# Optimization experiments

Measured on AMD Instinct MI355X. Metric: run time of the kernel, lower is better.

Reference implementation:

```python
import jax, jax.numpy as jnp
import numpy as np

QLEN, B, D, NH, DH, DI = 1024, 4, 1024, 16, 64, 4096
KLEN = QLEN
RLEN = QLEN + KLEN
EPS = 1e-12
SCALE = 1.0 / (DH ** 0.5)


def layer_norm(x, g, b):
    mu = jnp.mean(x, axis=-1, keepdims=True)
    var = jnp.mean(jnp.square(x - mu), axis=-1, keepdims=True)
    return (x - mu) * jax.lax.rsqrt(var + EPS) * g + b


def rel_shift(x, klen):
    # x: [qlen, rlen, b, n] -> [qlen, klen, b, n] via XLNet reshape trick
    q, r_, b, n = x.shape
    x = jnp.reshape(x, (r_, q, b, n))[1:]
    x = jnp.reshape(x, (q, r_ - 1, b, n))[:, :klen]
    return x


def setup_inputs() -> dict:
    key = jax.random.key(0)
    ks = jax.random.split(key, 16)
    std = 0.02
    h = jax.random.normal(ks[0], (QLEN, B, D), jnp.float32)
    r = jax.random.normal(ks[1], (RLEN, B, D), jnp.float32)
    # causal mask: 1 where key position j > query position i (disallowed)
    m = (jnp.arange(KLEN)[None, :] > jnp.arange(QLEN)[:, None]).astype(jnp.float32)
    attn_mask = jnp.broadcast_to(m[:, :, None, None], (QLEN, KLEN, B, 1))
    # segment matrix: one-hot of (seg_i != seg_j), shape [q, k, b, 2]
    seg_ids = jax.random.randint(ks[2], (QLEN, B), 0, 2)
    diff = (seg_ids[:, None, :] != seg_ids[None, :, :]).astype(jnp.int32)
    seg_mat = jax.nn.one_hot(diff, 2, dtype=jnp.float32)
    p = lambda k, shape: jax.random.normal(k, shape, jnp.float32) * std
    return {
        'h': h, 'r': r, 'attn_mask': attn_mask, 'seg_mat': seg_mat,
        'q_w': p(ks[3], (D, NH, DH)), 'k_w': p(ks[4], (D, NH, DH)),
        'v_w': p(ks[5], (D, NH, DH)), 'o_w': p(ks[6], (D, NH, DH)),
        'r_w': p(ks[7], (D, NH, DH)),
        'r_r_bias': jnp.zeros((NH, DH), jnp.float32),
        'r_s_bias': jnp.zeros((NH, DH), jnp.float32),
        'r_w_bias': jnp.zeros((NH, DH), jnp.float32),
        'seg_embed': p(ks[8], (2, NH, DH)),
        'ln1_g': jnp.ones((D,), jnp.float32), 'ln1_b': jnp.zeros((D,), jnp.float32),
        'ff_w1': p(ks[9], (D, DI)), 'ff_b1': jnp.zeros((DI,), jnp.float32),
        'ff_w2': p(ks[10], (DI, D)), 'ff_b2': jnp.zeros((D,), jnp.float32),
        'ln2_g': jnp.ones((D,), jnp.float32), 'ln2_b': jnp.zeros((D,), jnp.float32),
    }


def reference(h, r, attn_mask, seg_mat, q_w, k_w, v_w, o_w, r_w,
              r_r_bias, r_s_bias, r_w_bias, seg_embed,
              ln1_g, ln1_b, ff_w1, ff_b1, ff_w2, ff_b2, ln2_g, ln2_b):
    # projections (single-stream: g=None, mems=None => cat == h)
    q_head = jnp.einsum('ibh,hnd->ibnd', h, q_w)
    k_head = jnp.einsum('ibh,hnd->ibnd', h, k_w)
    v_head = jnp.einsum('ibh,hnd->ibnd', h, v_w)
    k_r = jnp.einsum('ibh,hnd->ibnd', r, r_w)
    # content + relative position + segment bias terms
    ac = jnp.einsum('ibnd,jbnd->ijbn', q_head + r_w_bias, k_head)
    bd = jnp.einsum('ibnd,jbnd->ijbn', q_head + r_r_bias, k_r)
    bd = rel_shift(bd, KLEN)
    ef = jnp.einsum('ibnd,snd->ibns', q_head + r_s_bias, seg_embed)
    ef = jnp.einsum('ijbs,ibns->ijbn', seg_mat, ef)
    attn_score = (ac + bd + ef) * SCALE - 1e30 * attn_mask
    attn_prob = jax.nn.softmax(attn_score, axis=1)
    attn_vec = jnp.einsum('ijbn,jbnd->ibnd', attn_prob, v_head)
    # post-attention
    attn_out = jnp.einsum('ibnd,hnd->ibh', attn_vec, o_w) + h
    out = layer_norm(attn_out, ln1_g, ln1_b)
    # feed-forward
    ff = jax.nn.gelu(jnp.einsum('ibh,hf->ibf', out, ff_w1) + ff_b1, approximate=False)
    ff = jnp.einsum('ibf,fh->ibh', ff, ff_w2) + ff_b2
    return layer_norm(ff + out, ln2_g, ln2_b)
```

## Files before the change

kernel.cpp:

```cpp
#include <hip/hip_runtime.h>
#include <hip/hip_bf16.h>

using bf16 = __hip_bfloat16;
typedef __attribute__((ext_vector_type(8))) short short8;
typedef __attribute__((ext_vector_type(4))) float floatx4;

#define QLEN 1024
#define KLEN 1024
#define RLEN 2048
#define RUSED 1152
#define BB   4
#define DMODEL 1024
#define NH   16
#define DH   64
#define DI   4096
#define ND   1024
#define QKVS 3072
#define SCALE 0.125f

__device__ inline void gl_lds16(const bf16* g, bf16* l) {
  __builtin_amdgcn_global_load_lds(
      (__attribute__((address_space(1))) void*)(g),
      (__attribute__((address_space(3))) void*)(l), 16, 0, 0);
}

__global__ __launch_bounds__(256) void cvt_all(
    const float* __restrict__ h, const float* __restrict__ r,
    const float* __restrict__ ow,
    bf16* __restrict__ hb, bf16* __restrict__ rb, bf16* __restrict__ wo)
{
  const int id = blockIdx.x;
  const float* src; bf16* dst; int off;
  if (id < 2048)      { src = h;  dst = hb; off = id * 2048; }
  else if (id < 4352) { src = r;  dst = rb; off = (id - 2048) * 2048; }
  else                { src = ow; dst = wo; off = (id - 4352) * 2048; }
  const int idx = off + threadIdx.x * 8;
  const float4 a = *reinterpret_cast<const float4*>(src + idx);
  const float4 b = *reinterpret_cast<const float4*>(src + idx + 4);
  bf16 o[8] = {__float2bfloat16(a.x), __float2bfloat16(a.y),
               __float2bfloat16(a.z), __float2bfloat16(a.w),
               __float2bfloat16(b.x), __float2bfloat16(b.y),
               __float2bfloat16(b.z), __float2bfloat16(b.w)};
  *reinterpret_cast<uint4*>(dst + idx) = *reinterpret_cast<uint4*>(o);
}

__device__ inline void tconv_tile(const float* __restrict__ src, bf16* __restrict__ dst,
                                  int R, int C, int bx, int by, int tid) {
  __shared__ float tile[32][33];
  const int r0 = by * 32, c0 = bx * 32;
  {
    const int tr = tid >> 3, tc = (tid & 7) * 4;
    const float4 f = *reinterpret_cast<const float4*>(src + (size_t)(r0 + tr) * C + c0 + tc);
    tile[tr][tc + 0] = f.x; tile[tr][tc + 1] = f.y;
    tile[tr][tc + 2] = f.z; tile[tr][tc + 3] = f.w;
  }
  __syncthreads();
  {
    const int oc = tid >> 3, orr = (tid & 7) * 4;
    bf16 o[4];
#pragma unroll
    for (int u = 0; u < 4; ++u) o[u] = __float2bfloat16(tile[orr + u][oc]);
    *reinterpret_cast<uint2*>(dst + (size_t)(c0 + oc) * R + r0 + orr) = *reinterpret_cast<uint2*>(o);
  }
}

__global__ __launch_bounds__(256) void tconv_all(
    const float* __restrict__ qw, const float* __restrict__ kw,
    const float* __restrict__ vw, const float* __restrict__ rw,
    const float* __restrict__ w1, const float* __restrict__ w2,
    bf16* __restrict__ wqkvt, bf16* __restrict__ wrt,
    bf16* __restrict__ w1t, bf16* __restrict__ w2t)
{
  const int id = blockIdx.x;
  const int tid = threadIdx.x;
  if (id < 4096) {
    const int part = id >> 10, local = id & 1023;
    const float* src = (part == 0) ? qw : (part == 1) ? kw : (part == 2) ? vw : rw;
    bf16* dst = (part < 3) ? (wqkvt + (size_t)part * ND * DMODEL) : wrt;
    tconv_tile(src, dst, DMODEL, ND, local & 31, local >> 5, tid);
  } else if (id < 8192) {
    const int local = id - 4096;
    tconv_tile(w1, w1t, DMODEL, DI, local & 127, local >> 7, tid);
  } else {
    const int local = id - 8192;
    tconv_tile(w2, w2t, DI, DMODEL, local & 31, local >> 5, tid);
  }
}

__global__ __launch_bounds__(256) void seg_extract(const float* __restrict__ seg,
                                                   float* __restrict__ dsb) {
  const int idx = blockIdx.x * 256 + threadIdx.x;
  const int i = idx >> 2, b = idx & 3;
  dsb[b * QLEN + i] = seg[(size_t)(i * KLEN * BB + b) * 2 + 1];
}

__global__ __launch_bounds__(512, 4) void gemm256(
    const bf16* __restrict__ A, const bf16* __restrict__ Bt,
    int M, int N, int K, int Ktot, int lda, int ldb,
    const float* __restrict__ bias, int act_gelu,
    float* __restrict__ outf, bf16* __restrict__ outb, int pstride)
{
  __shared__ __attribute__((aligned(16))) bf16 As[2][128 * 64];
  __shared__ __attribute__((aligned(16))) bf16 Bs[2][128 * 64];

  const int tid = threadIdx.x;
  const int wave = tid >> 6, lane = tid & 63;

  const int gX = gridDim.x;
  const int nwg = gX * gridDim.y;
  int lin = blockIdx.y * gX + blockIdx.x;
  {
    const int q = nwg >> 3, r = nwg & 7;
    const int xcd = lin & 7, idx = lin >> 3;
    lin = (xcd < r ? xcd * (q + 1) : r * (q + 1) + (xcd - r) * q) + idx;
  }
  const int n0b = (lin % gX) << 7;
  const int m0b = (lin / gX) << 7;

  const int z = blockIdx.z;
  const int kbeg = z * K;
  const int nkt = min(K, Ktot - kbeg) >> 6;
  const bf16* Ab = A + (size_t)kbeg;
  const bf16* Bb = Bt + (size_t)kbeg;
  float* of = outf ? (outf + (size_t)z * pstride) : outf;
  bf16*  ob = outb ? (outb + (size_t)z * pstride) : outb;

  const int srow = lane >> 3;
  const int scol = ((lane & 7) ^ srow) << 3;
  const bf16* gA = Ab + (size_t)(m0b + wave * 8 + srow) * lda + scol;
  const bf16* gB = Bb + (size_t)(n0b + wave * 8 + srow) * ldb + scol;
  const int lofs = wave * (8 * 64) + lane * 8;
  bf16* lA[2] = {&As[0][lofs], &As[1][lofs]};
  bf16* lB[2] = {&Bs[0][lofs], &Bs[1][lofs]};

  const int fl = lane & 15, quad = lane >> 4;
  const int wm = (wave >> 2) * 64;
  const int wn = (wave & 3) * 32;
  const int ch0 = (quad ^ (fl & 7)) << 3;

  floatx4 acc[4][2];
#pragma unroll
  for (int mi = 0; mi < 4; ++mi)
#pragma unroll
    for (int ni = 0; ni < 2; ++ni) acc[mi][ni] = (floatx4){0.f, 0.f, 0.f, 0.f};

  {
    gl_lds16(gA, lA[0]);
    gl_lds16(gA + (size_t)64 * lda, lA[0] + 4096);
    gl_lds16(gB, lB[0]);
    gl_lds16(gB + (size_t)64 * ldb, lB[0] + 4096);
  }
  if (nkt > 1) {
    gl_lds16(gA + 64, lA[1]);
    gl_lds16(gA + (size_t)64 * lda + 64, lA[1] + 4096);
    gl_lds16(gB + 64, lB[1]);
    gl_lds16(gB + (size_t)64 * ldb + 64, lB[1] + 4096);
  }

  for (int kt = 0; kt < nkt; ++kt) {
    if (kt + 1 < nkt) {
      asm volatile("s_waitcnt vmcnt(4)" ::: "memory");
    } else {
      asm volatile("s_waitcnt vmcnt(0)" ::: "memory");
    }
    __builtin_amdgcn_s_barrier();
    __builtin_amdgcn_sched_barrier(0);

    const bf16* as = (kt & 1) ? &As[1][0] : &As[0][0];
    const bf16* bs = (kt & 1) ? &Bs[1][0] : &Bs[0][0];
#pragma unroll
    for (int ks = 0; ks < 2; ++ks) {
      const int ch = ch0 ^ (ks << 5);
      short8 af[4], bv[2];
#pragma unroll
      for (int mi = 0; mi < 4; ++mi)
        af[mi] = *reinterpret_cast<const short8*>(&as[(wm + mi * 16 + fl) * 64 + ch]);
#pragma unroll
      for (int ni = 0; ni < 2; ++ni)
        bv[ni] = *reinterpret_cast<const short8*>(&bs[(wn + ni * 16 + fl) * 64 + ch]);
      __builtin_amdgcn_s_setprio(1);
#pragma unroll
      for (int mi = 0; mi < 4; ++mi)
#pragma unroll
        for (int ni = 0; ni < 2; ++ni)
          acc[mi][ni] = __builtin_amdgcn_mfma_f32_16x16x32_bf16(af[mi], bv[ni], acc[mi][ni], 0, 0, 0);
      __builtin_amdgcn_s_setprio(0);
    }
    __builtin_amdgcn_sched_barrier(0);
    __builtin_amdgcn_s_barrier();
    if (kt + 2 < nkt) {
      const size_t ko = (size_t)(kt + 2) << 6;
      bf16* dA = (kt & 1) ? lA[1] : lA[0];
      bf16* dB = (kt & 1) ? lB[1] : lB[0];
      gl_lds16(gA + ko, dA);
      gl_lds16(gA + (size_t)64 * lda + ko, dA + 4096);
      gl_lds16(gB + ko, dB);
      gl_lds16(gB + (size_t)64 * ldb + ko, dB + 4096);
    }
  }

#pragma unroll
  for (int mi = 0; mi < 4; ++mi) {
#pragma unroll
    for (int r = 0; r < 4; ++r) {
      const int row = m0b + wm + mi * 16 + quad * 4 + r;
#pragma unroll
      for (int ni = 0; ni < 2; ++ni) {
        const int col = n0b + wn + ni * 16 + fl;
        float v = acc[mi][ni][r];
        if (bias) v += bias[col];
        if (act_gelu) v = 0.5f * v * (1.0f + erff(v * 0.70710678118654752f));
        const size_t idx = (size_t)row * N + col;
        if (of) of[idx] = v;
        else    ob[idx] = __float2bfloat16(v);
      }
    }
  }
}

__global__ __launch_bounds__(256, 3) void attn_kernel(
    const bf16* __restrict__ qkv, const bf16* __restrict__ kr,
    const float* __restrict__ dsb, const float* __restrict__ seg_embed,
    const float* __restrict__ rwb, const float* __restrict__ rrb,
    const float* __restrict__ rsb,
    bf16* __restrict__ av_out)
{
  const int bx = blockIdx.x;
  const int n  = bx & 15;
  const int b  = (bx >> 4) & 3;
  const int it = 15 - (bx >> 6);
  const int i0 = it * 64;
  const int tid = threadIdx.x;

  const bf16* qh = qkv + n * DH;
  const bf16* kh = qkv + ND + n * DH;
  const bf16* vh = qkv + 2 * ND + n * DH;

  __shared__ bf16 Kb[64][72];
  __shared__ bf16 VT[64][72];
  __shared__ bf16 krw[128][72];
  __shared__ bf16 bdrL[64][88];
  __shared__ float efs0[64], efs1[64];
  __shared__ float dsq[64], dsk[64];

  const int wave = tid >> 6, lane = tid & 63;
  const int fl = lane & 15, quad = lane >> 4;
  const int wq0 = wave * 16;
  const int tb0 = 3 - wave;
  const int twoc = (tid & 3) << 1;

  short8 aw[2], ar[2];
  {
    const int qrow = i0 + wq0 + fl;
    const bf16* qp = qh + (size_t)(qrow * BB + b) * QKVS;
    float e0 = 0.f, e1 = 0.f;
#pragma unroll
    for (int ks = 0; ks < 2; ++ks) {
      const int d0 = ks * 32 + quad * 8;
      const uint4 qv = *reinterpret_cast<const uint4*>(qp + d0);
      const bf16* qe = reinterpret_cast<const bf16*>(&qv);
      bf16 wt[8], rt[8];
#pragma unroll
      for (int u = 0; u < 8; ++u) {
        const int d = d0 + u;
        const float qf = __bfloat162float(qe[u]);
        wt[u] = __float2bfloat16(qf + rwb[n * DH + d]);
        rt[u] = __float2bfloat16(qf + rrb[n * DH + d]);
        const float qs = qf + rsb[n * DH + d];
        e0 += qs * seg_embed[(0 * NH + n) * DH + d];
        e1 += qs * seg_embed[(1 * NH + n) * DH + d];
      }
      aw[ks] = *reinterpret_cast<short8*>(wt);
      ar[ks] = *reinterpret_cast<short8*>(rt);
    }
    e0 += __shfl_xor(e0, 16, 64); e0 += __shfl_xor(e0, 32, 64);
    e1 += __shfl_xor(e1, 16, 64); e1 += __shfl_xor(e1, 32, 64);
    if (quad == 0) { efs0[wq0 + fl] = e0; efs1[wq0 + fl] = e1; }
    if (tid < 64) dsq[tid] = dsb[b * QLEN + i0 + tid];
  }

  floatx4 O[4];
#pragma unroll
  for (int nb = 0; nb < 4; ++nb) O[nb] = (floatx4){0.f, 0.f, 0.f, 0.f};
  float l_loc[4] = {0.f, 0.f, 0.f, 0.f};

  const int sj  = tid >> 2;
  const int sdc = (tid & 3) << 4;
  const int st  = tid >> 1;
  const int sdc2= (tid & 1) << 5;
  uint4 kv0, kv1, vv0, vv1, rr0, rr1, rr2, rr3;
  {
    const bf16* kp = kh + (size_t)((0 + sj) * BB + b) * QKVS + sdc;
    kv0 = reinterpret_cast<const uint4*>(kp)[0];
    kv1 = reinterpret_cast<const uint4*>(kp)[1];
    const bf16* vp = vh + (size_t)((0 + sj) * BB + b) * QKVS + sdc;
    vv0 = reinterpret_cast<const uint4*>(vp)[0];
    vv1 = reinterpret_cast<const uint4*>(vp)[1];
    const int kbase0 = QLEN - i0 - 63;
    const bf16* rp = kr + ((size_t)((kbase0 + st) * BB + b)) * ND + n * DH + sdc2;
    rr0 = reinterpret_cast<const uint4*>(rp)[0];
    rr1 = reinterpret_cast<const uint4*>(rp)[1];
    rr2 = reinterpret_cast<const uint4*>(rp)[2];
    rr3 = reinterpret_cast<const uint4*>(rp)[3];
  }

  for (int jt = 0; jt <= it; ++jt) {
    const int j0 = jt * 64;

    __syncthreads();

    {
      reinterpret_cast<uint4*>(&Kb[sj][sdc])[0] = kv0;
      reinterpret_cast<uint4*>(&Kb[sj][sdc + 8])[0] = kv1;
      const bf16* ve0 = reinterpret_cast<const bf16*>(&vv0);
      const bf16* ve1 = reinterpret_cast<const bf16*>(&vv1);
#pragma unroll
      for (int u = 0; u < 8; ++u) {
        VT[sdc + (u ^ twoc)][sj] = ve0[u];
        VT[sdc + 8 + (u ^ twoc)][sj] = ve1[u];
      }
      reinterpret_cast<uint4*>(&krw[st][sdc2 + 0])[0]  = rr0;
      reinterpret_cast<uint4*>(&krw[st][sdc2 + 8])[0]  = rr1;
      reinterpret_cast<uint4*>(&krw[st][sdc2 + 16])[0] = rr2;
      reinterpret_cast<uint4*>(&krw[st][sdc2 + 24])[0] = rr3;
      if (tid < 64) dsk[tid] = dsb[b * QLEN + j0 + tid];
    }

    if (jt < it) {
      const int j0n = j0 + 64;
      const bf16* kp = kh + (size_t)((j0n + sj) * BB + b) * QKVS + sdc;
      kv0 = reinterpret_cast<const uint4*>(kp)[0];
      kv1 = reinterpret_cast<const uint4*>(kp)[1];
      const bf16* vp = vh + (size_t)((j0n + sj) * BB + b) * QKVS + sdc;
      vv0 = reinterpret_cast<const uint4*>(vp)[0];
      vv1 = reinterpret_cast<const uint4*>(vp)[1];
      const int kbn = QLEN + j0n - i0 - 63;
      const bf16* rp = kr + ((size_t)((kbn + st) * BB + b)) * ND + n * DH + sdc2;
      rr0 = reinterpret_cast<const uint4*>(rp)[0];
      rr1 = reinterpret_cast<const uint4*>(rp)[1];
      rr2 = reinterpret_cast<const uint4*>(rp)[2];
      rr3 = reinterpret_cast<const uint4*>(rp)[3];
    }

    __syncthreads();

    floatx4 accS[4], accB[5];
#pragma unroll
    for (int nb = 0; nb < 4; ++nb) accS[nb] = (floatx4){0.f, 0.f, 0.f, 0.f};
#pragma unroll
    for (int u = 0; u < 5; ++u) accB[u] = (floatx4){0.f, 0.f, 0.f, 0.f};
#pragma unroll
    for (int ks = 0; ks < 2; ++ks) {
#pragma unroll
      for (int nb = 0; nb < 4; ++nb)
        accS[nb] = __builtin_amdgcn_mfma_f32_16x16x32_bf16(
            aw[ks], *reinterpret_cast<const short8*>(&Kb[nb * 16 + fl][ks * 32 + quad * 8]), accS[nb], 0, 0, 0);
#pragma unroll
      for (int u = 0; u < 5; ++u)
        accB[u] = __builtin_amdgcn_mfma_f32_16x16x32_bf16(
            ar[ks], *reinterpret_cast<const short8*>(&krw[(tb0 + u) * 16 + fl][ks * 32 + quad * 8]), accB[u], 0, 0, 0);
    }
#pragma unroll
    for (int u = 0; u < 5; ++u)
#pragma unroll
      for (int r = 0; r < 4; ++r)
        bdrL[wq0 + quad * 4 + r][u * 16 + fl] = __float2bfloat16(accB[u][r]);

    float pv[4][4];
#pragma unroll
    for (int r = 0; r < 4; ++r) {
      const int qL = wq0 + quad * 4 + r;
      const int qg = i0 + qL;
      const float e0q = efs0[qL], e1q = efs1[qL];
      const float dq = dsq[qL];
#pragma unroll
      for (int nb = 0; nb < 4; ++nb) {
        const int kL = nb * 16 + fl;
        const int kg = j0 + kL;
        const float bdv = __bfloat162float(bdrL[qL][15 + kL - quad * 4 - r]);
        const float ef = (dq != dsk[kL]) ? e1q : e0q;
        const float s = (accS[nb][r] + bdv + ef) * SCALE;
        const float pe = (kg > qg) ? 0.0f : __expf(s);
        pv[nb][r] = pe;
        l_loc[r] += pe;
      }
    }

#pragma unroll
    for (int nb = 0; nb < 4; ++nb)
#pragma unroll
      for (int r = 0; r < 4; ++r)
        bdrL[wq0 + quad * 4 + r][nb * 16 + fl] = __float2bfloat16(pv[nb][r]);

#pragma unroll
    for (int ks = 0; ks < 2; ++ks) {
      const short8 ap = *reinterpret_cast<const short8*>(&bdrL[wq0 + fl][ks * 32 + quad * 8]);
#pragma unroll
      for (int nb = 0; nb < 4; ++nb)
        O[nb] = __builtin_amdgcn_mfma_f32_16x16x32_bf16(
            ap, *reinterpret_cast<const short8*>(&VT[nb * 16 + (fl ^ (nb << 1))][ks * 32 + quad * 8]), O[nb], 0, 0, 0);
    }
  }

  float inv[4];
#pragma unroll
  for (int r = 0; r < 4; ++r) {
    float l = l_loc[r];
    l += __shfl_xor(l, 1, 64);
    l += __shfl_xor(l, 2, 64);
    l += __shfl_xor(l, 4, 64);
    l += __shfl_xor(l, 8, 64);
    inv[r] = 1.0f / l;
  }
#pragma unroll
  for (int r = 0; r < 4; ++r) {
    const int qL = wq0 + quad * 4 + r;
    bf16* op = av_out + ((size_t)((i0 + qL) * BB + b)) * ND + n * DH;
#pragma unroll
    for (int nb = 0; nb < 4; ++nb)
      op[nb * 16 + fl] = __float2bfloat16(O[nb][r] * inv[r]);
  }
}

__global__ __launch_bounds__(256) void ln_fused(
    const float* __restrict__ pa, const float* __restrict__ pb,
    const float* __restrict__ resid,
    const float* __restrict__ gg, const float* __restrict__ bbias,
    float* __restrict__ outf, bf16* __restrict__ outb)
{
  const int row = blockIdx.x;
  const int tid = threadIdx.x;
  __shared__ float red[4];
  const size_t base = (size_t)row * DMODEL;

  float v[4];
  float s = 0.0f;
#pragma unroll
  for (int k = 0; k < 4; ++k) {
    const int c = k * 256 + tid;
    const float x = pa[base + c] + pb[base + c] + resid[base + c];
    v[k] = x;
    s += x;
  }
#pragma unroll
  for (int off = 32; off; off >>= 1) s += __shfl_xor(s, off, 64);
  const int w = tid >> 6, lane = tid & 63;
  if (lane == 0) red[w] = s;
  __syncthreads();
  const float mean = (red[0] + red[1] + red[2] + red[3]) * (1.0f / DMODEL);

  float s2 = 0.0f;
#pragma unroll
  for (int k = 0; k < 4; ++k) {
    const float dlt = v[k] - mean;
    s2 += dlt * dlt;
  }
  __syncthreads();
#pragma unroll
  for (int off = 32; off; off >>= 1) s2 += __shfl_xor(s2, off, 64);
  if (lane == 0) red[w] = s2;
  __syncthreads();
  const float var = (red[0] + red[1] + red[2] + red[3]) * (1.0f / DMODEL);
  const float rstd = rsqrtf(var + 1e-12f);

#pragma unroll
  for (int k = 0; k < 4; ++k) {
    const int c = k * 256 + tid;
    const float o = (v[k] - mean) * rstd * gg[c] + bbias[c];
    if (outf) outf[base + c] = o;
    if (outb) outb[base + c] = __float2bfloat16(o);
  }
}

__global__ __launch_bounds__(256) void ln_fused2b(
    const bf16* __restrict__ pa, const bf16* __restrict__ pb,
    const float* __restrict__ resid, const float* __restrict__ bias,
    const float* __restrict__ gg, const float* __restrict__ bbias,
    float* __restrict__ outf)
{
  const int row = blockIdx.x;
  const int tid = threadIdx.x;
  __shared__ float red[4];
  const size_t base = (size_t)row * DMODEL;

  float v[4];
  float s = 0.0f;
#pragma unroll
  for (int k = 0; k < 4; ++k) {
    const int c = k * 256 + tid;
    float x = __bfloat162float(pa[base + c]) + __bfloat162float(pb[base + c]) +
              resid[base + c] + bias[c];
    v[k] = x;
    s += x;
  }
#pragma unroll
  for (int off = 32; off; off >>= 1) s += __shfl_xor(s, off, 64);
  const int w = tid >> 6, lane = tid & 63;
  if (lane == 0) red[w] = s;
  __syncthreads();
  const float mean = (red[0] + red[1] + red[2] + red[3]) * (1.0f / DMODEL);

  float s2 = 0.0f;
#pragma unroll
  for (int k = 0; k < 4; ++k) {
    const float dlt = v[k] - mean;
    s2 += dlt * dlt;
  }
  __syncthreads();
#pragma unroll
  for (int off = 32; off; off >>= 1) s2 += __shfl_xor(s2, off, 64);
  if (lane == 0) red[w] = s2;
  __syncthreads();
  const float var = (red[0] + red[1] + red[2] + red[3]) * (1.0f / DMODEL);
  const float rstd = rsqrtf(var + 1e-12f);

#pragma unroll
  for (int k = 0; k < 4; ++k) {
    const int c = k * 256 + tid;
    outf[base + c] = (v[k] - mean) * rstd * gg[c] + bbias[c];
  }
}

extern "C" void kernel_launch(void* const* d_in, const int* in_sizes, int n_in,
                              void* d_out, int out_size, void* d_ws, size_t ws_size,
                              hipStream_t stream) {
  const float* h         = (const float*)d_in[0];
  const float* r         = (const float*)d_in[1];
  const float* seg_mat   = (const float*)d_in[3];
  const float* q_w       = (const float*)d_in[4];
  const float* k_w       = (const float*)d_in[5];
  const float* v_w       = (const float*)d_in[6];
  const float* o_w       = (const float*)d_in[7];
  const float* r_w       = (const float*)d_in[8];
  const float* r_r_bias  = (const float*)d_in[9];
  const float* r_s_bias  = (const float*)d_in[10];
  const float* r_w_bias  = (const float*)d_in[11];
  const float* seg_embed = (const float*)d_in[12];
  const float* ln1_g     = (const float*)d_in[13];
  const float* ln1_b     = (const float*)d_in[14];
  const float* ff_w1     = (const float*)d_in[15];
  const float* ff_b1     = (const float*)d_in[16];
  const float* ff_w2     = (const float*)d_in[17];
  const float* ff_b2     = (const float*)d_in[18];
  const float* ln2_g     = (const float*)d_in[19];
  const float* ln2_b     = (const float*)d_in[20];
  float* outp = (float*)d_out;

  const size_t M1 = (size_t)QLEN * BB;
  const size_t MRU = (size_t)RUSED * BB;
  char* ws = (char*)d_ws;
  const size_t MB = 1u << 20;

  bf16* hb   = (bf16*)(ws + 0 * MB);
  bf16* rb   = (bf16*)(ws + 8 * MB);
  bf16* wqkvt= (bf16*)(ws + 24 * MB);
  bf16* wrt  = (bf16*)(ws + 30 * MB);
  bf16* wo   = (bf16*)(ws + 32 * MB);
  bf16* w1t  = (bf16*)(ws + 34 * MB);
  bf16* w2t  = (bf16*)(ws + 42 * MB);
  bf16* qkvb = (bf16*)(ws + 50 * MB);
  bf16* krb  = (bf16*)(ws + 74 * MB);
  bf16* avb  = (bf16*)(ws + 90 * MB);
  float* pa1  = (float*)(ws + 0 * MB);
  float* pb1  = (float*)(ws + 16 * MB);
  float* out1 = (float*)(ws + 50 * MB);
  bf16* out1b = (bf16*)(ws + 66 * MB);
  bf16* ff1   = (bf16*)(ws + 0 * MB);
  bf16* p2    = (bf16*)(ws + 74 * MB);
  float* dsbuf = (float*)(ws + 106 * MB);

  dim3 blk(256);
  dim3 blk512(512);

  cvt_all<<<dim3(4864), blk, 0, stream>>>(h, r, o_w, hb, rb, wo);
  tconv_all<<<dim3(12288), blk, 0, stream>>>(q_w, k_w, v_w, r_w, ff_w1, ff_w2,
                                             wqkvt, wrt, w1t, w2t);
  seg_extract<<<dim3(16), blk, 0, stream>>>(seg_mat, dsbuf);

  gemm256<<<dim3(QKVS / 128, M1 / 128, 1), blk512, 0, stream>>>(
      hb, wqkvt, (int)M1, QKVS, DMODEL, DMODEL, DMODEL, DMODEL, nullptr, 0, nullptr, qkvb, 0);
  gemm256<<<dim3(ND / 128, (int)(MRU / 128), 1), blk512, 0, stream>>>(
      rb, wrt, (int)MRU, ND, DMODEL, DMODEL, DMODEL, DMODEL, nullptr, 0, nullptr, krb, 0);

  attn_kernel<<<dim3(16 * BB * NH), blk, 0, stream>>>(
      qkvb, krb, dsbuf, seg_embed,
      r_w_bias, r_r_bias, r_s_bias, avb);

  gemm256<<<dim3(DMODEL / 128, M1 / 128, 2), blk512, 0, stream>>>(
      avb, wo, (int)M1, DMODEL, ND / 2, ND, ND, ND, nullptr, 0, pa1, nullptr, (int)(M1 * DMODEL));

  ln_fused<<<dim3((int)M1), blk, 0, stream>>>(pa1, pb1, h, ln1_g, ln1_b, out1, out1b);

  gemm256<<<dim3(DI / 128, M1 / 128, 1), blk512, 0, stream>>>(
      out1b, w1t, (int)M1, DI, DMODEL, DMODEL, DMODEL, DMODEL, ff_b1, 1, nullptr, ff1, 0);

  gemm256<<<dim3(DMODEL / 128, M1 / 128, 2), blk512, 0, stream>>>(
      ff1, w2t, (int)M1, DMODEL, DI / 2, DI, DI, DI, nullptr, 0, nullptr, p2, (int)(M1 * DMODEL));

  ln_fused2b<<<dim3((int)M1), blk, 0, stream>>>(
      p2, p2 + M1 * DMODEL,
      out1, ff_b2, ln2_g, ln2_b, outp);
}
```

Measured before the change: 432.0 us.

## Add 256x256-tile pipelined GEMM with XCD remap and split-K 4 for FF2

Adds a new GEMM kernel with 256x256 output tiles per 512-thread block. It loads operands straight into LDS in a multi-stage ping-pong pipeline with explicit waitcnt and barrier control, raises wave priority around the MFMA bursts, and remaps block indices across XCDs. This kernel replaces the 128-tile GEMM for the QKV, output-projection and both FFN matmuls, aiming for more data reuse per LDS load. The second FFN matmul now splits K four ways, and the final layernorm sums four bf16 partials instead of two. The trade-off is fewer blocks in flight (e.g. 192 or 128 blocks for some GEMMs), less occupancy, and more partial-sum traffic.

```diff
diff --git a/kernel.cpp b/kernel.cpp
--- a/kernel.cpp
+++ b/kernel.cpp
@@ -218,6 +218,133 @@
   }
 }
 
+__global__ __launch_bounds__(512, 2) void gemm8p(
+    const bf16* __restrict__ A, const bf16* __restrict__ Bt,
+    int M, int N, int K, int Ktot, int lda, int ldb,
+    const float* __restrict__ bias, int act_gelu,
+    float* __restrict__ outf, bf16* __restrict__ outb, int pstride)
+{
+  __shared__ __attribute__((aligned(16))) bf16 Asm[4 * 8192];
+  __shared__ __attribute__((aligned(16))) bf16 Bsm[4 * 8192];
+
+  const int tid = threadIdx.x;
+  const int wave = tid >> 6, lane = tid & 63;
+
+  const int gX = gridDim.x;
+  const int nwg = gX * gridDim.y;
+  int lin = blockIdx.y * gX + blockIdx.x;
+  {
+    const int q = nwg >> 3, r = nwg & 7;
+    const int xcd = lin & 7, idx = lin >> 3;
+    lin = (xcd < r ? xcd * (q + 1) : r * (q + 1) + (xcd - r) * q) + idx;
+  }
+  const int n0b = (lin % gX) << 8;
+  const int m0b = (lin / gX) << 8;
+
+  const int z = blockIdx.z;
+  const int kbeg = z * K;
+  const int nkt = min(K, Ktot - kbeg) >> 6;
+  float* of = outf ? (outf + (size_t)z * pstride) : outf;
+  bf16*  ob = outb ? (outb + (size_t)z * pstride) : outb;
+
+  const int srow = tid >> 2;
+  const int sswz = (((tid & 3) ^ (srow & 3)) << 3);
+  const bf16* Ar0 = A + (size_t)(m0b + srow) * lda + kbeg + sswz;
+  const bf16* Ar1 = Ar0 + (size_t)128 * lda;
+  const bf16* Br0 = Bt + (size_t)(n0b + srow) * ldb + kbeg + sswz;
+  const bf16* Br1 = Br0 + (size_t)128 * ldb;
+  bf16* lAd = Asm + tid * 8;
+  bf16* lBd = Bsm + tid * 8;
+#define STG_A(si, kcol) { gl_lds16(Ar0 + (kcol), lAd + (si) * 8192); \
+                          gl_lds16(Ar1 + (kcol), lAd + (si) * 8192 + 4096); }
+#define STG_B(si, kcol) { gl_lds16(Br0 + (kcol), lBd + (si) * 8192); \
+                          gl_lds16(Br1 + (kcol), lBd + (si) * 8192 + 4096); }
+
+  const int fl = lane & 15, quad = lane >> 4;
+  const int wr = wave >> 2, wc = wave & 3;
+  const int rch = (quad ^ (fl & 3)) << 3;
+  const int arow0 = wr * 128 + fl;
+  const int brow0 = wc * 64 + fl;
+
+  floatx4 acc[8][4];
+#pragma unroll
+  for (int mi = 0; mi < 8; ++mi)
+#pragma unroll
+    for (int ni = 0; ni < 4; ++ni) acc[mi][ni] = (floatx4){0.f, 0.f, 0.f, 0.f};
+
+  STG_A(0, 0); STG_B(0, 0);
+  STG_A(1, 32); STG_B(1, 32);
+  STG_A(2, 64); STG_B(2, 64);
+  asm volatile("s_waitcnt vmcnt(8)" ::: "memory");
+  __builtin_amdgcn_s_barrier();
+
+  short8 bv[4];
+  for (int j = 0; j < nkt; ++j) {
+    const int d = j & 1;
+    const int sbase = d * 2;
+#pragma unroll
+    for (int p = 0; p < 4; ++p) {
+      __builtin_amdgcn_sched_barrier(0);
+      const int kh = p >> 1, mih = p & 1;
+      const bf16* asl = Asm + (size_t)(sbase + kh) * 8192;
+      const bf16* bsl = Bsm + (size_t)(sbase + kh) * 8192;
+      short8 af[4];
+#pragma unroll
+      for (int i = 0; i < 4; ++i)
+        af[i] = *reinterpret_cast<const short8*>(asl + (arow0 + (mih * 4 + i) * 16) * 32 + rch);
+      if (mih == 0) {
+#pragma unroll
+        for (int nn = 0; nn < 4; ++nn)
+          bv[nn] = *reinterpret_cast<const short8*>(bsl + (brow0 + nn * 16) * 32 + rch);
+      }
+      if (p == 0 && j + 1 < nkt) STG_A(((d ^ 1) * 2 + 1), (size_t)(j + 1) * 64 + 32);
+      if (p == 1 && j + 1 < nkt) STG_B(((d ^ 1) * 2 + 1), (size_t)(j + 1) * 64 + 32);
+      if (p == 2 && j + 2 < nkt) STG_A((d * 2), (size_t)(j + 2) * 64);
+      if (p == 3 && j + 2 < nkt) STG_B((d * 2), (size_t)(j + 2) * 64);
+      if (p == 1) {
+        if (j == nkt - 1) { asm volatile("s_waitcnt vmcnt(0)" ::: "memory"); }
+        else              { asm volatile("s_waitcnt vmcnt(8)" ::: "memory"); }
+      }
+      if (p == 3 && j < nkt - 1) {
+        if (j == nkt - 2) { asm volatile("s_waitcnt vmcnt(4)" ::: "memory"); }
+        else              { asm volatile("s_waitcnt vmcnt(8)" ::: "memory"); }
+      }
+      __builtin_amdgcn_s_barrier();
+      __builtin_amdgcn_sched_barrier(0);
+      __builtin_amdgcn_s_setprio(1);
+#pragma unroll
+      for (int i = 0; i < 4; ++i)
+#pragma unroll
+        for (int nn = 0; nn < 4; ++nn)
+          acc[mih * 4 + i][nn] = __builtin_amdgcn_mfma_f32_16x16x32_bf16(
+              af[i], bv[nn], acc[mih * 4 + i][nn], 0, 0, 0);
+      __builtin_amdgcn_s_setprio(0);
+      __builtin_amdgcn_sched_barrier(0);
+      __builtin_amdgcn_s_barrier();
+    }
+  }
+#undef STG_A
+#undef STG_B
+
+#pragma unroll
+  for (int mi = 0; mi < 8; ++mi) {
+#pragma unroll
+    for (int r = 0; r < 4; ++r) {
+      const int row = m0b + wr * 128 + mi * 16 + quad * 4 + r;
+#pragma unroll
+      for (int ni = 0; ni < 4; ++ni) {
+        const int col = n0b + wc * 64 + ni * 16 + fl;
+        float v = acc[mi][ni][r];
+        if (bias) v += bias[col];
+        if (act_gelu) v = 0.5f * v * (1.0f + erff(v * 0.70710678118654752f));
+        const size_t idx = (size_t)row * N + col;
+        if (of) of[idx] = v;
+        else    ob[idx] = __float2bfloat16(v);
+      }
+    }
+  }
+}
+
 __global__ __launch_bounds__(256, 3) void attn_kernel(
     const bf16* __restrict__ qkv, const bf16* __restrict__ kr,
     const float* __restrict__ dsb, const float* __restrict__ seg_embed,
@@ -472,8 +599,9 @@
   }
 }
 
-__global__ __launch_bounds__(256) void ln_fused2b(
+__global__ __launch_bounds__(256) void ln_fused4b(
     const bf16* __restrict__ pa, const bf16* __restrict__ pb,
+    const bf16* __restrict__ pc, const bf16* __restrict__ pd,
     const float* __restrict__ resid, const float* __restrict__ bias,
     const float* __restrict__ gg, const float* __restrict__ bbias,
     float* __restrict__ outf)
@@ -489,6 +617,7 @@
   for (int k = 0; k < 4; ++k) {
     const int c = k * 256 + tid;
     float x = __bfloat162float(pa[base + c]) + __bfloat162float(pb[base + c]) +
+              __bfloat162float(pc[base + c]) + __bfloat162float(pd[base + c]) +
               resid[base + c] + bias[c];
     v[k] = x;
     s += x;
@@ -577,7 +706,7 @@
                                              wqkvt, wrt, w1t, w2t);
   seg_extract<<<dim3(16), blk, 0, stream>>>(seg_mat, dsbuf);
 
-  gemm256<<<dim3(QKVS / 128, M1 / 128, 1), blk512, 0, stream>>>(
+  gemm8p<<<dim3(QKVS / 256, M1 / 256, 1), blk512, 0, stream>>>(
       hb, wqkvt, (int)M1, QKVS, DMODEL, DMODEL, DMODEL, DMODEL, nullptr, 0, nullptr, qkvb, 0);
   gemm256<<<dim3(ND / 128, (int)(MRU / 128), 1), blk512, 0, stream>>>(
       rb, wrt, (int)MRU, ND, DMODEL, DMODEL, DMODEL, DMODEL, nullptr, 0, nullptr, krb, 0);
@@ -586,18 +715,18 @@
       qkvb, krb, dsbuf, seg_embed,
       r_w_bias, r_r_bias, r_s_bias, avb);
 
-  gemm256<<<dim3(DMODEL / 128, M1 / 128, 2), blk512, 0, stream>>>(
+  gemm8p<<<dim3(DMODEL / 256, M1 / 256, 2), blk512, 0, stream>>>(
       avb, wo, (int)M1, DMODEL, ND / 2, ND, ND, ND, nullptr, 0, pa1, nullptr, (int)(M1 * DMODEL));
 
   ln_fused<<<dim3((int)M1), blk, 0, stream>>>(pa1, pb1, h, ln1_g, ln1_b, out1, out1b);
 
-  gemm256<<<dim3(DI / 128, M1 / 128, 1), blk512, 0, stream>>>(
+  gemm8p<<<dim3(DI / 256, M1 / 256, 1), blk512, 0, stream>>>(
       out1b, w1t, (int)M1, DI, DMODEL, DMODEL, DMODEL, DMODEL, ff_b1, 1, nullptr, ff1, 0);
 
-  gemm256<<<dim3(DMODEL / 128, M1 / 128, 2), blk512, 0, stream>>>(
-      ff1, w2t, (int)M1, DMODEL, DI / 2, DI, DI, DI, nullptr, 0, nullptr, p2, (int)(M1 * DMODEL));
-
-  ln_fused2b<<<dim3((int)M1), blk, 0, stream>>>(
-      p2, p2 + M1 * DMODEL,
+  gemm8p<<<dim3(DMODEL / 256, M1 / 256, 4), blk512, 0, stream>>>(
+      ff1, w2t, (int)M1, DMODEL, DI / 4, DI, DI, DI, nullptr, 0, nullptr, p2, (int)(M1 * DMODEL));
+
+  ln_fused4b<<<dim3((int)M1), blk, 0, stream>>>(
+      p2, p2 + M1 * DMODEL, p2 + 2 * M1 * DMODEL, p2 + 3 * M1 * DMODEL,
       out1, ff_b2, ln2_g, ln2_b, outp);
 }
```

After: 488.7 us. 13.1% more time.
